# Optimization experiments

Hardware: AMD Instinct MI355X
Metric: run time of the kernel (lower is better)

Reference implementation:

```python
import jax, jax.numpy as jnp
import numpy as np
import math

B, T, D = 4, 1024, 512
H, HD = 8, 64
FF = 2048
L = 2
MEM = 512
S = T + MEM  # src length
EPS = 1e-5


def _sinusoid(positions, dim):
    pos = positions.astype(jnp.float32)[:, None]                      # [P,1]
    div = jnp.exp(jnp.arange(0, dim, 2, dtype=jnp.float32) * (-math.log(10000.0) / dim))
    enc = jnp.zeros((positions.shape[0], dim), jnp.float32)
    enc = enc.at[:, 0::2].set(jnp.sin(pos * div))
    enc = enc.at[:, 1::2].set(jnp.cos(pos * div))
    return enc


def _layer_norm(x, scale, bias):
    m = jnp.mean(x, axis=-1, keepdims=True)
    v = jnp.var(x, axis=-1, keepdims=True)
    return (x - m) / jnp.sqrt(v + EPS) * scale + bias


def _rel_shift(x):
    # x: [T, S, B, H] -> Transformer-XL relative shift
    t, s, b, h = x.shape
    xp = jnp.concatenate([jnp.zeros((t, 1, b, h), x.dtype), x], axis=1)  # [T,S+1,B,H]
    xp = xp.reshape(s + 1, t, b, h)
    return xp[1:].reshape(t, s, b, h)


def setup_inputs() -> dict:
    key = jax.random.key(0)
    ks = jax.random.split(key, 16)
    w = 0.02
    inp = {
        "x": jax.random.normal(ks[0], (B, T, D), jnp.float32),
        "positions": jnp.arange(S - 1, -1, -1, dtype=jnp.int64 if jax.config.jax_enable_x64 else jnp.int32),
        # causal-with-memory mask: query i (src position i+MEM) cannot see src j > i + MEM
        "attn_mask": jnp.arange(S)[None, :] > (jnp.arange(T)[:, None] + MEM),
        "mems": jax.random.normal(ks[1], (L + 1, MEM, B, D), jnp.float32) * 0.5,
        "u_bias": jax.random.normal(ks[2], (H, HD), jnp.float32) * w,
        "v_bias": jax.random.normal(ks[3], (H, HD), jnp.float32) * w,
        "qkv_w": jax.random.normal(ks[4], (L, 3 * H * HD, D), jnp.float32) * w,
        "pos_w": jax.random.normal(ks[5], (L, H * HD, D), jnp.float32) * w,
        "out_w": jax.random.normal(ks[6], (L, D, H * HD), jnp.float32) * w,
        "lin1_w": jax.random.normal(ks[7], (L, FF, D), jnp.float32) * w,
        "lin1_b": jnp.zeros((L, FF), jnp.float32),
        "lin2_w": jax.random.normal(ks[8], (L, D, FF), jnp.float32) * w,
        "lin2_b": jnp.zeros((L, D), jnp.float32),
        "ln1_s": jnp.ones((L, D), jnp.float32),
        "ln1_b": jnp.zeros((L, D), jnp.float32),
        "ln2_s": jnp.ones((L, D), jnp.float32),
        "ln2_b": jnp.zeros((L, D), jnp.float32),
    }
    return inp


def reference(x, positions, attn_mask, mems, u_bias, v_bias, qkv_w, pos_w, out_w,
              lin1_w, lin1_b, lin2_w, lin2_b, ln1_s, ln1_b, ln2_s, ln2_b):
    scale = 1.0 / math.sqrt(D)  # source uses 1/sqrt(embed_dim)
    xs = jnp.swapaxes(x, 0, 1)                       # [T,B,D] (batch_first -> time-first)
    pe = _sinusoid(positions, D)                     # [S,D]
    out = xs
    hiddens = [xs]
    for l in range(L):
        cat = jnp.concatenate([mems[l], out], axis=0)            # [S,B,D]
        qkv = jnp.einsum('sbd,ed->sbe', cat, qkv_w[l])           # [S,B,3*H*HD]
        q, k, v = jnp.split(qkv, 3, axis=-1)
        q = q[-T:].reshape(T, B, H, HD)
        k = k.reshape(S, B, H, HD)
        v = v.reshape(S, B, H, HD)
        r = jnp.einsum('sd,ed->se', pe, pos_w[l]).reshape(S, H, HD)
        content = jnp.einsum('ibnd,jbnd->ijbn', q + u_bias, k)   # [T,S,B,H]
        pos_sc = jnp.einsum('ibnd,jnd->ijbn', q + v_bias, r)     # [T,S,B,H]
        score = (content + _rel_shift(pos_sc)) * scale
        score = jnp.where(attn_mask[:, :, None, None], -jnp.inf, score)
        attn = jax.nn.softmax(score, axis=1)
        ctx = jnp.einsum('ijbn,jbnd->ibnd', attn, v).reshape(T, B, H * HD)
        a_out = jnp.einsum('tbe,de->tbd', ctx, out_w[l])
        h = _layer_norm(out + a_out, ln1_s[l], ln1_b[l])
        ff = jnp.einsum('tbf,df->tbd', jax.nn.relu(jnp.einsum('tbd,fd->tbf', h, lin1_w[l]) + lin1_b[l]), lin2_w[l]) + lin2_b[l]
        out = _layer_norm(h + ff, ln2_s[l], ln2_b[l])
        hiddens.append(out)
    final = jnp.swapaxes(out[-T:], 0, 1)             # [B,T,D]
    new_mems = jax.lax.stop_gradient(jnp.stack(
        [jnp.concatenate([mems[i], hiddens[i]], axis=0)[-MEM:] for i in range(L + 1)], axis=0))
    return final, new_mems
```

## Files before the change

### kernel.cpp

```cpp
#include <hip/hip_runtime.h>

constexpr int BB = 4, TT = 1024, DD = 512, HH = 8, HDIM = 64;
constexpr int FFD = 2048, NLAYER = 2, MM = 512, SS = 1536;
constexpr float LN_EPS = 1e-5f;
constexpr float SCALE = 0.04419417382415922f;

typedef unsigned short u16;
typedef __attribute__((ext_vector_type(8))) short bf16x8;
typedef __attribute__((ext_vector_type(4))) float f32x4;

__device__ __forceinline__ float b2f(u16 u) {
  union { unsigned int i; float f; } c; c.i = ((unsigned int)u) << 16; return c.f;
}
__device__ __forceinline__ u16 f2b(float f) {
  unsigned int x = __builtin_bit_cast(unsigned int, f);
  x += 0x7fffu + ((x >> 16) & 1u);
  return (u16)(x >> 16);
}

__device__ __forceinline__ void dma16(const u16* g, u16* l) {
  __builtin_amdgcn_global_load_lds(
      (const __attribute__((address_space(1))) unsigned int*)g,
      (__attribute__((address_space(3))) unsigned int*)l, 16, 0, 0);
}

constexpr int OFF_X    = 0;
constexpr int OFF_MEMS = 2097152;
constexpr int OFF_UB   = 5242880;
constexpr int OFF_VB   = 5243392;
constexpr int OFF_QKVW = 5243904;
constexpr int OFF_POSW = 6816768;
constexpr int OFF_OUTW = 7341056;
constexpr int OFF_L1W  = 7865344;
constexpr int OFF_L1B  = 9962496;
constexpr int OFF_L2W  = 9966592;
constexpr int OFF_L2B  = 12063744;
constexpr int OFF_LN1S = 12064768;
constexpr int OFF_LN1B = 12065792;
constexpr int OFF_LN2S = 12066816;
constexpr int OFF_LN2B = 12067840;
constexpr int TOT_IN   = 12068864;
constexpr int PE_CNT   = SS * 256;

__global__ void txl_probe(const u16* __restrict__ xr, int* __restrict__ flag) {
  int lane = threadIdx.x;
  int cnt = 0;
  for (int k = 0; k < 8; ++k) {
    u16 u = xr[lane * 8 + k];
    int e = (u >> 7) & 0xFF;
    if (e >= 0xC0) ++cnt;
  }
  for (int o = 32; o; o >>= 1) cnt += __shfl_xor(cnt, o);
  if (lane == 0) *flag = (cnt >= 32) ? 1 : 0;
}

__global__ __launch_bounds__(256) void txl_convert(
    const void* x, const void* mems, const void* ub, const void* vb,
    const void* qkvw, const void* posw, const void* outw,
    const void* l1w, const void* l1b, const void* l2w, const void* l2b,
    const void* ln1s, const void* ln1b, const void* ln2s, const void* ln2b,
    u16* __restrict__ dst, u16* __restrict__ pe, const int* __restrict__ flag) {
  int idx = blockIdx.x * 256 + threadIdx.x;
  if (idx >= TOT_IN) {
    int idx2 = idx - TOT_IN;
    if (idx2 >= PE_CNT) return;
    int p = idx2 >> 8, m = idx2 & 255;
    float posf = (float)(SS - 1 - p);
    float div = expf((float)(2 * m) * (-9.210340371976184f / 512.0f));
    float a = posf * div;
    pe[(size_t)p * DD + 2 * m] = f2b(sinf(a));
    pe[(size_t)p * DD + 2 * m + 1] = f2b(cosf(a));
    return;
  }
  const void* p; int local;
  if      (idx < OFF_MEMS) { p = x;    local = idx; }
  else if (idx < OFF_UB)   { p = mems; local = idx - OFF_MEMS; }
  else if (idx < OFF_VB)   { p = ub;   local = idx - OFF_UB; }
  else if (idx < OFF_QKVW) { p = vb;   local = idx - OFF_VB; }
  else if (idx < OFF_POSW) { p = qkvw; local = idx - OFF_QKVW; }
  else if (idx < OFF_OUTW) { p = posw; local = idx - OFF_POSW; }
  else if (idx < OFF_L1W)  { p = outw; local = idx - OFF_OUTW; }
  else if (idx < OFF_L1B)  { p = l1w;  local = idx - OFF_L1W; }
  else if (idx < OFF_L2W)  { p = l1b;  local = idx - OFF_L1B; }
  else if (idx < OFF_L2B)  { p = l2w;  local = idx - OFF_L2W; }
  else if (idx < OFF_LN1S) { p = l2b;  local = idx - OFF_L2B; }
  else if (idx < OFF_LN1B) { p = ln1s; local = idx - OFF_LN1S; }
  else if (idx < OFF_LN2S) { p = ln1b; local = idx - OFF_LN1B; }
  else if (idx < OFF_LN2B) { p = ln2s; local = idx - OFF_LN2S; }
  else                     { p = ln2b; local = idx - OFF_LN2B; }
  dst[idx] = (*flag) ? f2b(((const float*)p)[local]) : ((const u16*)p)[local];
}

template <int EPI>
__global__ __launch_bounds__(256) void txl_gemm4(const u16* __restrict__ A,
                                                 const u16* __restrict__ B,
                                                 float* __restrict__ C,
                                                 u16* __restrict__ Obf,
                                                 const u16* __restrict__ bias,
                                                 int M, int N, int K, int KS) {
  __shared__ __align__(16) u16 As[2][128 * 32];
  __shared__ __align__(16) u16 Bs[2][128 * 32];
  const int tid = threadIdx.x;
  const int wave = tid >> 6, lane = tid & 63;
  const int wm = (wave & 1) * 64, wn = (wave >> 1) * 64;
  const int m0 = blockIdx.x * 128, n0 = blockIdx.y * 128;
  const int kbeg = blockIdx.z * KS, kend = kbeg + KS;
  const int L15 = lane & 15, quad = lane >> 4;

  auto stage = [&](int k0, int buf) {
    for (int c = 0; c < 2; ++c) {
      int segBase = c * 256 + wave * 64;
      int seg = segBase + lane;
      int row = seg >> 2, q = seg & 3;
      dma16(&A[(size_t)(m0 + row) * K + k0 + q * 8], &As[buf][segBase * 8]);
      dma16(&B[(size_t)(n0 + row) * K + k0 + q * 8], &Bs[buf][segBase * 8]);
    }
  };

  f32x4 acc[4][4] = {};
  stage(kbeg, 0);
  __syncthreads();
  int buf = 0;
  for (int k0 = kbeg; k0 < kend; k0 += 32) {
    if (k0 + 32 < kend) stage(k0 + 32, buf ^ 1);
    bf16x8 af[4], bfr[4];
    for (int t = 0; t < 4; ++t)
      af[t] = *reinterpret_cast<const bf16x8*>(&As[buf][(wm + t * 16 + L15) * 32 + quad * 8]);
    for (int t = 0; t < 4; ++t)
      bfr[t] = *reinterpret_cast<const bf16x8*>(&Bs[buf][(wn + t * 16 + L15) * 32 + quad * 8]);
    for (int tm = 0; tm < 4; ++tm)
      for (int tn = 0; tn < 4; ++tn)
        acc[tm][tn] = __builtin_amdgcn_mfma_f32_16x16x32_bf16(af[tm], bfr[tn], acc[tm][tn], 0, 0, 0);
    buf ^= 1;
    __syncthreads();
  }
  float* Cz = C + (size_t)blockIdx.z * ((size_t)M * N);
#pragma unroll
  for (int tm = 0; tm < 4; ++tm)
#pragma unroll
    for (int tn = 0; tn < 4; ++tn) {
      int col = n0 + wn + tn * 16 + L15;
#pragma unroll
      for (int r = 0; r < 4; ++r) {
        int row = m0 + wm + tm * 16 + quad * 4 + r;
        if (EPI == 0) {
          Cz[(size_t)row * N + col] = acc[tm][tn][r];
        } else {
          float v = acc[tm][tn][r] + b2f(bias[col]);
          Obf[(size_t)row * N + col] = f2b(fmaxf(v, 0.f));
        }
      }
    }
}

__global__ __launch_bounds__(256) void txl_gemm_r(const u16* __restrict__ A,
                                                  const u16* __restrict__ B,
                                                  u16* __restrict__ rb,
                                                  int M, int N, int K) {
  __shared__ __align__(16) u16 As[2][128 * 32];
  __shared__ __align__(16) u16 Bs[2][128 * 32];
  const int tid = threadIdx.x;
  const int wave = tid >> 6, lane = tid & 63;
  const int wm = (wave & 1) * 64, wn = (wave >> 1) * 64;
  const int m0 = blockIdx.x * 128, n0 = blockIdx.y * 128;
  const int L15 = lane & 15, quad = lane >> 4;

  auto stage = [&](int k0, int buf) {
    for (int c = 0; c < 2; ++c) {
      int segBase = c * 256 + wave * 64;
      int seg = segBase + lane;
      int row = seg >> 2, q = seg & 3;
      dma16(&A[(size_t)(m0 + row) * K + k0 + q * 8], &As[buf][segBase * 8]);
      dma16(&B[(size_t)(n0 + row) * K + k0 + q * 8], &Bs[buf][segBase * 8]);
    }
  };

  f32x4 acc[4][4] = {};
  stage(0, 0);
  __syncthreads();
  int buf = 0;
  for (int k0 = 0; k0 < K; k0 += 32) {
    if (k0 + 32 < K) stage(k0 + 32, buf ^ 1);
    bf16x8 af[4], bfr[4];
    for (int t = 0; t < 4; ++t)
      af[t] = *reinterpret_cast<const bf16x8*>(&As[buf][(wm + t * 16 + L15) * 32 + quad * 8]);
    for (int t = 0; t < 4; ++t)
      bfr[t] = *reinterpret_cast<const bf16x8*>(&Bs[buf][(wn + t * 16 + L15) * 32 + quad * 8]);
    for (int tm = 0; tm < 4; ++tm)
      for (int tn = 0; tn < 4; ++tn)
        acc[tm][tn] = __builtin_amdgcn_mfma_f32_16x16x32_bf16(af[tm], bfr[tn], acc[tm][tn], 0, 0, 0);
    buf ^= 1;
    __syncthreads();
  }
#pragma unroll
  for (int tm = 0; tm < 4; ++tm)
#pragma unroll
    for (int tn = 0; tn < 4; ++tn) {
      int col = n0 + wn + tn * 16 + L15;
      int n = col >> 6, d = col & 63;
#pragma unroll
      for (int r = 0; r < 4; ++r) {
        int row = m0 + wm + tm * 16 + quad * 4 + r;
        rb[((size_t)n * SS + row) * HDIM + d] = f2b(acc[tm][tn][r]);
      }
    }
}

__global__ void txl_transpose_in(const u16* __restrict__ x, u16* __restrict__ cur_bf,
                                 float* __restrict__ cur_f, void* __restrict__ outv,
                                 const int* __restrict__ flag) {
  int idx = blockIdx.x * 256 + threadIdx.x;
  if (idx >= BB * TT * DD) return;
  int b = idx >> 19, t = (idx >> 9) & 1023, d = idx & 511;
  u16 v = x[idx];
  size_t o = ((size_t)t * BB + b) * DD + d;
  cur_bf[o] = v; cur_f[o] = b2f(v);
  if (t >= 512) {
    size_t mo = 2097152 + (o - 1048576);
    if (*flag) ((float*)outv)[mo] = b2f(v);
    else       ((u16*)outv)[mo] = v;
  }
}

__global__ __launch_bounds__(256) void txl_qkv_scatter(
    const float* __restrict__ C, const u16* __restrict__ ub, const u16* __restrict__ vb,
    u16* __restrict__ qu, u16* __restrict__ qv, u16* __restrict__ kb) {
  size_t idx = (size_t)blockIdx.x * 256 + threadIdx.x;
  if (idx >= (size_t)SS * BB * 1536) return;
  int e = (int)(idx % 1536);
  if (e >= 1024) return;
  int row = (int)(idx / 1536);
  int s = row >> 2, b = row & 3;
  float val = C[idx];
  if (e < 512) {
    if (s >= MM) {
      int i = s - MM, n = e >> 6, d = e & 63;
      size_t o = ((size_t)(b * HH + n) * TT + i) * HDIM + d;
      qu[o] = f2b(val + b2f(ub[e]));
      qv[o] = f2b(val + b2f(vb[e]));
    }
  } else {
    int e2 = e - 512, n = e2 >> 6, d = e2 & 63;
    kb[((size_t)(b * HH + n) * SS + s) * HDIM + d] = f2b(val);
  }
}

__global__ __launch_bounds__(256) void txl_v_transpose(const float* __restrict__ C,
                                                       u16* __restrict__ vT) {
  __shared__ u16 t[64][68];
  int bx = blockIdx.x;
  int sb = bx >> 5;
  int bn = bx & 31;
  int n = bn & 7, b = bn >> 3;
  int tid = threadIdx.x;
  int s0 = sb * 64;
  {
    int d = tid & 63, sr = tid >> 6;
    for (int i = 0; i < 16; ++i) {
      int s = s0 + sr + i * 4;
      t[sr + i * 4][d] = f2b(C[(size_t)(s * 4 + b) * 1536 + 1024 + n * 64 + d]);
    }
  }
  __syncthreads();
  {
    int s = tid & 63, dr = tid >> 6;
    u16* dst = vT + (size_t)(b * HH + n) * HDIM * SS;
    for (int i = 0; i < 16; ++i) {
      int d2 = dr + i * 4;
      dst[(size_t)d2 * SS + s0 + s] = t[s][d2];
    }
  }
}

__global__ __launch_bounds__(256) void txl_attn9(
    const u16* __restrict__ qu, const u16* __restrict__ qv, const u16* __restrict__ kbuf,
    const u16* __restrict__ vT, const u16* __restrict__ rbuf,
    float* __restrict__ O0, float* __restrict__ O1,
    float* __restrict__ L0, float* __restrict__ L1) {
  __shared__ __align__(16) u16 Kb[2][2048];
  __shared__ __align__(16) u16 Vb[2][2048];
  __shared__ __align__(16) u16 Rr[8][1024];
  __shared__ __align__(16) u16 ps4[4][640];

  const int bx = blockIdx.x;
  const int n = bx & 7;
  const int rest = bx >> 3;
  const int b = rest & 3;
  const int rest2 = rest >> 2;
  const int piece = rest2 >> 4;
  const int st = piece ? (15 - (rest2 & 15)) : (rest2 & 15);
  const int i0b = st * 64;
  const int g0 = 63 - (i0b >> 4);
  const int jcEnd = 18 + 2 * st;
  const int half = 9 + st;
  const int jcBeg = piece ? half : 0;
  const int jcLim = piece ? jcEnd : half;
  const int gB = g0 + 2 * jcBeg;

  const int tid = threadIdx.x, w = tid >> 6, lane = tid & 63;
  const int L15 = lane & 15, quad = lane >> 4;
  const int i0w = i0b + 16 * w;
  const int bh = b * HH + n;

  const u16* kB = kbuf + (size_t)bh * SS * HDIM;
  const u16* rB = rbuf + (size_t)n * SS * HDIM;
  const u16* vB = vT + (size_t)bh * HDIM * SS;

  const u16* quB = qu + ((size_t)bh * TT + i0w) * HDIM;
  const u16* qvB = qv + ((size_t)bh * TT + i0w) * HDIM;
  bf16x8 aqu[2], aqv[2];
  for (int c = 0; c < 2; ++c) {
    aqu[c] = *reinterpret_cast<const bf16x8*>(&quB[(size_t)L15 * HDIM + c * 32 + quad * 8]);
    aqv[c] = *reinterpret_cast<const bf16x8*>(&qvB[(size_t)L15 * HDIM + c * 32 + quad * 8]);
  }

  u16* ps = &ps4[w][0];

  auto stageK = [&](int jc) {
    const u16* src = kB + (size_t)(jc * 32 + (lane & 31)) * HDIM + (2 * w + (lane >> 5)) * 8;
    dma16(src, &Kb[jc & 1][512 * w]);
  };
  auto stageV = [&](int jc) {
    const u16* src = vB + (size_t)lane * SS + jc * 32 + 8 * w;
    dma16(src, &Vb[jc & 1][512 * w]);
  };
  auto stageRslab = [&](int slab) {
    int rrow = slab * 16 + (lane & 15);
    rrow = (rrow > SS - 1) ? (SS - 1) : rrow;
    const u16* s0 = rB + (size_t)rrow * HDIM + (lane >> 4) * 8;
    dma16(s0, &Rr[slab & 7][0]);
    dma16(s0 + 32, &Rr[slab & 7][512]);
  };
  auto rfrag = [&](int slab, int h) {
    return *reinterpret_cast<const bf16x8*>(&Rr[slab & 7][((quad + 4 * h) * 16 + L15) * 8]);
  };

  stageK(jcBeg); stageV(jcBeg);
  stageRslab(gB - 3 + w);
  if (w < 2) stageRslab(gB + 1 + w);
  __syncthreads();

  f32x4 pT0 = {};
  pT0 = __builtin_amdgcn_mfma_f32_16x16x32_bf16(aqv[0], rfrag(gB - w, 0), pT0, 0, 0, 0);
  pT0 = __builtin_amdgcn_mfma_f32_16x16x32_bf16(aqv[1], rfrag(gB - w, 1), pT0, 0, 0, 0);

  float l_lane[4] = {0.f, 0.f, 0.f, 0.f};
  f32x4 Oacc[4] = {};

  for (int jc = jcBeg; jc < jcLim; ++jc) {
    if (jc + 1 < jcLim) {
      stageK(jc + 1); stageV(jc + 1);
      if (w < 2) stageRslab(g0 + 3 + 2 * jc + w);
    }
    const int hslot = jc & 1, j0 = jc * 32;
    bf16x8 k00 = *reinterpret_cast<const bf16x8*>(&Kb[hslot][((quad) * 32 + L15) * 8]);
    bf16x8 k01 = *reinterpret_cast<const bf16x8*>(&Kb[hslot][((quad + 4) * 32 + L15) * 8]);
    bf16x8 k10 = *reinterpret_cast<const bf16x8*>(&Kb[hslot][((quad) * 32 + 16 + L15) * 8]);
    bf16x8 k11 = *reinterpret_cast<const bf16x8*>(&Kb[hslot][((quad + 4) * 32 + 16 + L15) * 8]);
    f32x4 s0v = {}, s1v = {};
    s0v = __builtin_amdgcn_mfma_f32_16x16x32_bf16(aqu[0], k00, s0v, 0, 0, 0);
    s0v = __builtin_amdgcn_mfma_f32_16x16x32_bf16(aqu[1], k01, s0v, 0, 0, 0);
    s1v = __builtin_amdgcn_mfma_f32_16x16x32_bf16(aqu[0], k10, s1v, 0, 0, 0);
    s1v = __builtin_amdgcn_mfma_f32_16x16x32_bf16(aqu[1], k11, s1v, 0, 0, 0);
    const int sl1 = g0 - w + 2 * jc + 1;
    f32x4 pT1 = {}, pT2 = {};
    pT1 = __builtin_amdgcn_mfma_f32_16x16x32_bf16(aqv[0], rfrag(sl1, 0), pT1, 0, 0, 0);
    pT1 = __builtin_amdgcn_mfma_f32_16x16x32_bf16(aqv[1], rfrag(sl1, 1), pT1, 0, 0, 0);
    pT2 = __builtin_amdgcn_mfma_f32_16x16x32_bf16(aqv[0], rfrag(sl1 + 1, 0), pT2, 0, 0, 0);
    pT2 = __builtin_amdgcn_mfma_f32_16x16x32_bf16(aqv[1], rfrag(sl1 + 1, 1), pT2, 0, 0, 0);
    for (int r = 0; r < 4; ++r) {
      int ii = quad * 4 + r;
      int i = i0w + ii;
      int c = 15 + L15 - ii;
      int srcLane = (quad << 4) | (c & 15);
      float a0 = __shfl(pT0[r], srcLane);
      float a1 = __shfl(pT1[r], srcLane);
      float b1v = __shfl(pT2[r], srcLane);
      float sv0 = s0v[r] + ((c < 16) ? a0 : a1);
      float sv1 = s1v[r] + ((c < 16) ? a1 : b1v);
      sv0 = (j0 + L15 <= i + MM) ? sv0 : -3e38f;
      sv1 = (j0 + 16 + L15 <= i + MM) ? sv1 : -3e38f;
      float e0 = __expf(sv0 * SCALE);
      float e1 = __expf(sv1 * SCALE);
      l_lane[r] += e0 + e1;
      int row = ii * 40;
      ps[row + L15] = f2b(e0);
      ps[row + 16 + L15] = f2b(e1);
    }
    bf16x8 ap = *reinterpret_cast<const bf16x8*>(&ps[L15 * 40 + quad * 8]);
    bf16x8 v0 = *reinterpret_cast<const bf16x8*>(&Vb[hslot][(quad * 64 + L15) * 8]);
    bf16x8 v1 = *reinterpret_cast<const bf16x8*>(&Vb[hslot][(quad * 64 + 16 + L15) * 8]);
    bf16x8 v2 = *reinterpret_cast<const bf16x8*>(&Vb[hslot][(quad * 64 + 32 + L15) * 8]);
    bf16x8 v3 = *reinterpret_cast<const bf16x8*>(&Vb[hslot][(quad * 64 + 48 + L15) * 8]);
    Oacc[0] = __builtin_amdgcn_mfma_f32_16x16x32_bf16(ap, v0, Oacc[0], 0, 0, 0);
    Oacc[1] = __builtin_amdgcn_mfma_f32_16x16x32_bf16(ap, v1, Oacc[1], 0, 0, 0);
    Oacc[2] = __builtin_amdgcn_mfma_f32_16x16x32_bf16(ap, v2, Oacc[2], 0, 0, 0);
    Oacc[3] = __builtin_amdgcn_mfma_f32_16x16x32_bf16(ap, v3, Oacc[3], 0, 0, 0);
    pT0 = pT2;
    __syncthreads();
  }

  float lsum[4];
  for (int r = 0; r < 4; ++r) {
    float s = l_lane[r];
    for (int o = 1; o < 16; o <<= 1) s += __shfl_xor(s, o);
    lsum[r] = s;
  }
  float* Op = piece ? O1 : O0;
  float* Lp = piece ? L1 : L0;
  for (int tn = 0; tn < 4; ++tn)
    for (int r = 0; r < 4; ++r) {
      int ii = quad * 4 + r;
      Op[((size_t)(i0w + ii) * BB + b) * DD + n * HDIM + tn * 16 + L15] = Oacc[tn][r];
    }
  if (L15 == 0)
    for (int r = 0; r < 4; ++r)
      Lp[(size_t)bh * TT + i0w + quad * 4 + r] = lsum[r];
}

__global__ void txl_attn_merge(const float* __restrict__ O0, const float* __restrict__ O1,
                               const float* __restrict__ L0, const float* __restrict__ L1,
                               u16* __restrict__ ctx) {
  int o = blockIdx.x * 256 + threadIdx.x;
  if (o >= BB * TT * DD) return;
  int i = o >> 11, b = (o >> 9) & 3, e = o & 511, n = e >> 6;
  size_t li = (size_t)(b * HH + n) * TT + i;
  float l = L0[li] + L1[li];
  ctx[o] = f2b((O0[o] + O1[o]) / l);
}

__global__ __launch_bounds__(256) void txl_ln(
    const float* __restrict__ gout, int nparts, const u16* __restrict__ bias,
    const float* __restrict__ resid, const u16* __restrict__ gam, const u16* __restrict__ bet,
    u16* __restrict__ ybf, float* __restrict__ yf,
    void* __restrict__ outv, int off, void* __restrict__ finalv,
    const int* __restrict__ flag) {
  const int row = blockIdx.x, tid = threadIdx.x;
  const int lane = tid & 63, wave = tid >> 6;
  __shared__ float red[4];
  size_t base = (size_t)row * DD;
  float x0 = resid[base + tid];
  float x1 = resid[base + tid + 256];
  for (int p = 0; p < nparts; ++p) {
    x0 += gout[(size_t)p * 2097152 + base + tid];
    x1 += gout[(size_t)p * 2097152 + base + tid + 256];
  }
  if (bias) { x0 += b2f(bias[tid]); x1 += b2f(bias[tid + 256]); }
  float s = x0 + x1;
  for (int o = 32; o; o >>= 1) s += __shfl_xor(s, o);
  if (lane == 0) red[wave] = s;
  __syncthreads();
  float mean = (red[0] + red[1] + red[2] + red[3]) * (1.f / DD);
  __syncthreads();
  float d0 = x0 - mean, d1 = x1 - mean;
  float q = d0 * d0 + d1 * d1;
  for (int o = 32; o; o >>= 1) q += __shfl_xor(q, o);
  if (lane == 0) red[wave] = q;
  __syncthreads();
  float var = (red[0] + red[1] + red[2] + red[3]) * (1.f / DD);
  float rstd = rsqrtf(var + LN_EPS);
  float y0 = d0 * rstd * b2f(gam[tid]) + b2f(bet[tid]);
  float y1 = d1 * rstd * b2f(gam[tid + 256]) + b2f(bet[tid + 256]);
  u16 u0 = f2b(y0), u1 = f2b(y1);
  ybf[base + tid] = u0;
  ybf[base + tid + 256] = u1;
  yf[base + tid] = y0;
  yf[base + tid + 256] = y1;
  if (outv && row >= 2048) {
    size_t mo = (size_t)off + (size_t)(row - 2048) * DD;
    if (*flag) {
      ((float*)outv)[mo + tid] = y0;
      ((float*)outv)[mo + tid + 256] = y1;
    } else {
      ((u16*)outv)[mo + tid] = u0;
      ((u16*)outv)[mo + tid + 256] = u1;
    }
  }
  if (finalv) {
    int t = row >> 2, b = row & 3;
    size_t fo = ((size_t)b * TT + t) * DD;
    if (*flag) {
      ((float*)finalv)[fo + tid] = y0;
      ((float*)finalv)[fo + tid + 256] = y1;
    } else {
      ((u16*)finalv)[fo + tid] = u0;
      ((u16*)finalv)[fo + tid + 256] = u1;
    }
  }
}

constexpr size_t WS_CUR_F  = 0;
constexpr size_t WS_CAT    = 8388608;
constexpr size_t WS_CBUF   = 14680064;
constexpr size_t WS_QU     = 52428800;
constexpr size_t WS_QV     = 56623104;
constexpr size_t WS_K      = 60817408;
constexpr size_t WS_VT     = 67108864;
constexpr size_t WS_R      = 73400320;
constexpr size_t WS_PE     = 74973184;
constexpr size_t WS_CTX    = 76546048;
constexpr size_t WS_HBF    = 80740352;
constexpr size_t WS_HF     = 84934656;
constexpr size_t WS_FF1    = 93323264;
constexpr size_t WS_CURBF  = 110100480;
constexpr size_t WS_CIN    = 114294784;
constexpr size_t WS_FLAG   = 138432512;
constexpr size_t WS_TOTAL  = 138432576;
constexpr size_t WS_OB0 = WS_CBUF;
constexpr size_t WS_OB1 = WS_CBUF + 8388608;
constexpr size_t WS_LB0 = WS_CBUF + 16777216;
constexpr size_t WS_LB1 = WS_CBUF + 16908288;

extern "C" void kernel_launch(void* const* d_in, const int* in_sizes, int n_in,
                              void* d_out, int out_size, void* d_ws, size_t ws_size,
                              hipStream_t stream) {
  (void)in_sizes; (void)n_in;

  if (ws_size < WS_TOTAL) {
    hipMemsetAsync(d_out, 0, (size_t)out_size * 2, stream);
    return;
  }
  char* ws = (char*)d_ws;
  float* cur_f  = (float*)(ws + WS_CUR_F);
  u16*   cat    = (u16*)(ws + WS_CAT);
  float* Cbuf   = (float*)(ws + WS_CBUF);
  float* Ob0    = (float*)(ws + WS_OB0);
  float* Ob1    = (float*)(ws + WS_OB1);
  float* Lb0    = (float*)(ws + WS_LB0);
  float* Lb1    = (float*)(ws + WS_LB1);
  u16*   qu     = (u16*)(ws + WS_QU);
  u16*   qv     = (u16*)(ws + WS_QV);
  u16*   kb     = (u16*)(ws + WS_K);
  u16*   vT     = (u16*)(ws + WS_VT);
  u16*   rb     = (u16*)(ws + WS_R);
  u16*   pe     = (u16*)(ws + WS_PE);
  u16*   ctx    = (u16*)(ws + WS_CTX);
  u16*   hbf    = (u16*)(ws + WS_HBF);
  float* hf     = (float*)(ws + WS_HF);
  u16*   ff1    = (u16*)(ws + WS_FF1);
  u16*   cur_bf = (u16*)(ws + WS_CURBF);
  u16*   cin    = (u16*)(ws + WS_CIN);
  int*   flag   = (int*)(ws + WS_FLAG);

  txl_probe<<<1, 64, 0, stream>>>((const u16*)d_in[0], flag);
  txl_convert<<<48680, 256, 0, stream>>>(
      d_in[0], d_in[3], d_in[4], d_in[5], d_in[6], d_in[7], d_in[8],
      d_in[9], d_in[10], d_in[11], d_in[12], d_in[13], d_in[14], d_in[15], d_in[16],
      cin, pe, flag);

  const u16* ub = cin + OFF_UB;
  const u16* vb = cin + OFF_VB;

  txl_transpose_in<<<8192, 256, 0, stream>>>(cin + OFF_X, cur_bf, cur_f, d_out, flag);

  for (int l = 0; l < NLAYER; ++l) {
    hipMemcpyAsync(cat, cin + OFF_MEMS + (size_t)l * 1048576, 2097152,
                   hipMemcpyDeviceToDevice, stream);
    hipMemcpyAsync(cat + 1048576, cur_bf, 4194304, hipMemcpyDeviceToDevice, stream);
    txl_gemm4<0><<<dim3(48, 12, 1), 256, 0, stream>>>(
        cat, cin + OFF_QKVW + (size_t)l * 786432, Cbuf, nullptr, nullptr, 6144, 1536, 512, 512);
    txl_qkv_scatter<<<36864, 256, 0, stream>>>(Cbuf, ub, vb, qu, qv, kb);
    txl_v_transpose<<<768, 256, 0, stream>>>(Cbuf, vT);
    txl_gemm_r<<<dim3(12, 4), 256, 0, stream>>>(
        pe, cin + OFF_POSW + (size_t)l * 262144, rb, 1536, 512, 512);
    txl_attn9<<<1024, 256, 0, stream>>>(qu, qv, kb, vT, rb, Ob0, Ob1, Lb0, Lb1);
    txl_attn_merge<<<8192, 256, 0, stream>>>(Ob0, Ob1, Lb0, Lb1, ctx);
    txl_gemm4<0><<<dim3(32, 4, 2), 256, 0, stream>>>(
        ctx, cin + OFF_OUTW + (size_t)l * 262144, Cbuf, nullptr, nullptr, 4096, 512, 512, 256);
    txl_ln<<<4096, 256, 0, stream>>>(Cbuf, 2, nullptr, cur_f,
                                     cin + OFF_LN1S + l * 512, cin + OFF_LN1B + l * 512,
                                     hbf, hf, nullptr, 0, nullptr, flag);
    txl_gemm4<1><<<dim3(32, 16, 1), 256, 0, stream>>>(
        hbf, cin + OFF_L1W + (size_t)l * 1048576, nullptr, ff1,
        cin + OFF_L1B + l * 2048, 4096, 2048, 512, 512);
    txl_gemm4<0><<<dim3(32, 4, 4), 256, 0, stream>>>(
        ff1, cin + OFF_L2W + (size_t)l * 1048576, Cbuf, nullptr, nullptr, 4096, 512, 2048, 512);
    txl_ln<<<4096, 256, 0, stream>>>(Cbuf, 4, cin + OFF_L2B + l * 512, hf,
                                     cin + OFF_LN2S + l * 512, cin + OFF_LN2B + l * 512,
                                     cur_bf, cur_f, d_out, 2097152 + (l + 1) * 1048576,
                                     (l == NLAYER - 1) ? d_out : nullptr, flag);
  }
}
```

Before: 476.0 us.

## Drop concat copies, batch positional GEMMs, merge QKV scatter with V transpose

The QKV GEMM now reads its A operand from two base pointers (memory rows, then current hidden rows), so the two device-to-device copies that built the concatenated buffer are removed. The positional projection for both layers is computed once up front in a single launch using a z grid dimension. The QKV scatter and V transpose kernels are merged into one launch that also skips the unused V columns in the scatter part. Together these cut launches and memory traffic, at the cost of a larger rel-pos buffer and extra pointer selection in the GEMM.

```diff
diff --git a/kernel.cpp b/kernel.cpp
--- a/kernel.cpp
+++ b/kernel.cpp
@@ -93,6 +93,7 @@
 
 template <int EPI>
 __global__ __launch_bounds__(256) void txl_gemm4(const u16* __restrict__ A,
+                                                 const u16* __restrict__ A2, int msplit,
                                                  const u16* __restrict__ B,
                                                  float* __restrict__ C,
                                                  u16* __restrict__ Obf,
@@ -106,13 +107,14 @@
   const int m0 = blockIdx.x * 128, n0 = blockIdx.y * 128;
   const int kbeg = blockIdx.z * KS, kend = kbeg + KS;
   const int L15 = lane & 15, quad = lane >> 4;
+  const u16* Abase = (m0 < msplit) ? (A + (size_t)m0 * K) : (A2 + (size_t)(m0 - msplit) * K);
 
   auto stage = [&](int k0, int buf) {
     for (int c = 0; c < 2; ++c) {
       int segBase = c * 256 + wave * 64;
       int seg = segBase + lane;
       int row = seg >> 2, q = seg & 3;
-      dma16(&A[(size_t)(m0 + row) * K + k0 + q * 8], &As[buf][segBase * 8]);
+      dma16(&Abase[(size_t)row * K + k0 + q * 8], &As[buf][segBase * 8]);
       dma16(&B[(size_t)(n0 + row) * K + k0 + q * 8], &Bs[buf][segBase * 8]);
     }
   };
@@ -164,6 +166,8 @@
   const int wm = (wave & 1) * 64, wn = (wave >> 1) * 64;
   const int m0 = blockIdx.x * 128, n0 = blockIdx.y * 128;
   const int L15 = lane & 15, quad = lane >> 4;
+  const u16* Bz = B + (size_t)blockIdx.z * 262144;
+  u16* rbz = rb + (size_t)blockIdx.z * 786432;
 
   auto stage = [&](int k0, int buf) {
     for (int c = 0; c < 2; ++c) {
@@ -171,7 +175,7 @@
       int seg = segBase + lane;
       int row = seg >> 2, q = seg & 3;
       dma16(&A[(size_t)(m0 + row) * K + k0 + q * 8], &As[buf][segBase * 8]);
-      dma16(&B[(size_t)(n0 + row) * K + k0 + q * 8], &Bs[buf][segBase * 8]);
+      dma16(&Bz[(size_t)(n0 + row) * K + k0 + q * 8], &Bs[buf][segBase * 8]);
     }
   };
 
@@ -201,7 +205,7 @@
 #pragma unroll
       for (int r = 0; r < 4; ++r) {
         int row = m0 + wm + tm * 16 + quad * 4 + r;
-        rb[((size_t)n * SS + row) * HDIM + d] = f2b(acc[tm][tn][r]);
+        rbz[((size_t)n * SS + row) * HDIM + d] = f2b(acc[tm][tn][r]);
       }
     }
 }
@@ -222,16 +226,40 @@
   }
 }
 
-__global__ __launch_bounds__(256) void txl_qkv_scatter(
+__global__ __launch_bounds__(256) void txl_qkv_post(
     const float* __restrict__ C, const u16* __restrict__ ub, const u16* __restrict__ vb,
-    u16* __restrict__ qu, u16* __restrict__ qv, u16* __restrict__ kb) {
-  size_t idx = (size_t)blockIdx.x * 256 + threadIdx.x;
-  if (idx >= (size_t)SS * BB * 1536) return;
-  int e = (int)(idx % 1536);
-  if (e >= 1024) return;
-  int row = (int)(idx / 1536);
+    u16* __restrict__ qu, u16* __restrict__ qv, u16* __restrict__ kb,
+    u16* __restrict__ vT) {
+  __shared__ u16 t[64][68];
+  const int bx = blockIdx.x;
+  const int tid = threadIdx.x;
+  if (bx < 768) {
+    int sb = bx >> 5;
+    int bn = bx & 31;
+    int n = bn & 7, b = bn >> 3;
+    int s0 = sb * 64;
+    {
+      int d = tid & 63, sr = tid >> 6;
+      for (int i = 0; i < 16; ++i) {
+        int s = s0 + sr + i * 4;
+        t[sr + i * 4][d] = f2b(C[(size_t)(s * 4 + b) * 1536 + 1024 + n * 64 + d]);
+      }
+    }
+    __syncthreads();
+    {
+      int s = tid & 63, dr = tid >> 6;
+      u16* dst = vT + (size_t)(b * HH + n) * HDIM * SS;
+      for (int i = 0; i < 16; ++i) {
+        int d2 = dr + i * 4;
+        dst[(size_t)d2 * SS + s0 + s] = t[s][d2];
+      }
+    }
+    return;
+  }
+  int idx = (bx - 768) * 256 + tid;
+  int row = idx >> 10, e = idx & 1023;
   int s = row >> 2, b = row & 3;
-  float val = C[idx];
+  float val = C[(size_t)row * 1536 + e];
   if (e < 512) {
     if (s >= MM) {
       int i = s - MM, n = e >> 6, d = e & 63;
@@ -242,33 +270,6 @@
   } else {
     int e2 = e - 512, n = e2 >> 6, d = e2 & 63;
     kb[((size_t)(b * HH + n) * SS + s) * HDIM + d] = f2b(val);
-  }
-}
-
-__global__ __launch_bounds__(256) void txl_v_transpose(const float* __restrict__ C,
-                                                       u16* __restrict__ vT) {
-  __shared__ u16 t[64][68];
-  int bx = blockIdx.x;
-  int sb = bx >> 5;
-  int bn = bx & 31;
-  int n = bn & 7, b = bn >> 3;
-  int tid = threadIdx.x;
-  int s0 = sb * 64;
-  {
-    int d = tid & 63, sr = tid >> 6;
-    for (int i = 0; i < 16; ++i) {
-      int s = s0 + sr + i * 4;
-      t[sr + i * 4][d] = f2b(C[(size_t)(s * 4 + b) * 1536 + 1024 + n * 64 + d]);
-    }
-  }
-  __syncthreads();
-  {
-    int s = tid & 63, dr = tid >> 6;
-    u16* dst = vT + (size_t)(b * HH + n) * HDIM * SS;
-    for (int i = 0; i < 16; ++i) {
-      int d2 = dr + i * 4;
-      dst[(size_t)d2 * SS + s0 + s] = t[s][d2];
-    }
   }
 }
 
@@ -490,7 +491,7 @@
 }
 
 constexpr size_t WS_CUR_F  = 0;
-constexpr size_t WS_CAT    = 8388608;
+constexpr size_t WS_RB2    = 8388608;
 constexpr size_t WS_CBUF   = 14680064;
 constexpr size_t WS_QU     = 52428800;
 constexpr size_t WS_QV     = 56623104;
@@ -522,7 +523,7 @@
   }
   char* ws = (char*)d_ws;
   float* cur_f  = (float*)(ws + WS_CUR_F);
-  u16*   cat    = (u16*)(ws + WS_CAT);
+  u16*   rb2    = (u16*)(ws + WS_RB2);
   float* Cbuf   = (float*)(ws + WS_CBUF);
   float* Ob0    = (float*)(ws + WS_OB0);
   float* Ob1    = (float*)(ws + WS_OB1);
@@ -532,7 +533,6 @@
   u16*   qv     = (u16*)(ws + WS_QV);
   u16*   kb     = (u16*)(ws + WS_K);
   u16*   vT     = (u16*)(ws + WS_VT);
-  u16*   rb     = (u16*)(ws + WS_R);
   u16*   pe     = (u16*)(ws + WS_PE);
   u16*   ctx    = (u16*)(ws + WS_CTX);
   u16*   hbf    = (u16*)(ws + WS_HBF);
@@ -551,30 +551,30 @@
   const u16* ub = cin + OFF_UB;
   const u16* vb = cin + OFF_VB;
 
+  txl_gemm_r<<<dim3(12, 4, 2), 256, 0, stream>>>(
+      pe, cin + OFF_POSW, rb2, 1536, 512, 512);
   txl_transpose_in<<<8192, 256, 0, stream>>>(cin + OFF_X, cur_bf, cur_f, d_out, flag);
 
   for (int l = 0; l < NLAYER; ++l) {
-    hipMemcpyAsync(cat, cin + OFF_MEMS + (size_t)l * 1048576, 2097152,
-                   hipMemcpyDeviceToDevice, stream);
-    hipMemcpyAsync(cat + 1048576, cur_bf, 4194304, hipMemcpyDeviceToDevice, stream);
     txl_gemm4<0><<<dim3(48, 12, 1), 256, 0, stream>>>(
-        cat, cin + OFF_QKVW + (size_t)l * 786432, Cbuf, nullptr, nullptr, 6144, 1536, 512, 512);
-    txl_qkv_scatter<<<36864, 256, 0, stream>>>(Cbuf, ub, vb, qu, qv, kb);
-    txl_v_transpose<<<768, 256, 0, stream>>>(Cbuf, vT);
-    txl_gemm_r<<<dim3(12, 4), 256, 0, stream>>>(
-        pe, cin + OFF_POSW + (size_t)l * 262144, rb, 1536, 512, 512);
-    txl_attn9<<<1024, 256, 0, stream>>>(qu, qv, kb, vT, rb, Ob0, Ob1, Lb0, Lb1);
+        cin + OFF_MEMS + (size_t)l * 1048576, cur_bf, 2048,
+        cin + OFF_QKVW + (size_t)l * 786432, Cbuf, nullptr, nullptr, 6144, 1536, 512, 512);
+    txl_qkv_post<<<25344, 256, 0, stream>>>(Cbuf, ub, vb, qu, qv, kb, vT);
+    txl_attn9<<<1024, 256, 0, stream>>>(qu, qv, kb, vT, rb2 + (size_t)l * 786432,
+                                        Ob0, Ob1, Lb0, Lb1);
     txl_attn_merge<<<8192, 256, 0, stream>>>(Ob0, Ob1, Lb0, Lb1, ctx);
     txl_gemm4<0><<<dim3(32, 4, 2), 256, 0, stream>>>(
-        ctx, cin + OFF_OUTW + (size_t)l * 262144, Cbuf, nullptr, nullptr, 4096, 512, 512, 256);
+        ctx, ctx, 1 << 30, cin + OFF_OUTW + (size_t)l * 262144, Cbuf,
+        nullptr, nullptr, 4096, 512, 512, 256);
     txl_ln<<<4096, 256, 0, stream>>>(Cbuf, 2, nullptr, cur_f,
                                      cin + OFF_LN1S + l * 512, cin + OFF_LN1B + l * 512,
                                      hbf, hf, nullptr, 0, nullptr, flag);
     txl_gemm4<1><<<dim3(32, 16, 1), 256, 0, stream>>>(
-        hbf, cin + OFF_L1W + (size_t)l * 1048576, nullptr, ff1,
-        cin + OFF_L1B + l * 2048, 4096, 2048, 512, 512);
+        hbf, hbf, 1 << 30, cin + OFF_L1W + (size_t)l * 1048576, nullptr,
+        ff1, cin + OFF_L1B + l * 2048, 4096, 2048, 512, 512);
     txl_gemm4<0><<<dim3(32, 4, 4), 256, 0, stream>>>(
-        ff1, cin + OFF_L2W + (size_t)l * 1048576, Cbuf, nullptr, nullptr, 4096, 512, 2048, 512);
+        ff1, ff1, 1 << 30, cin + OFF_L2W + (size_t)l * 1048576, Cbuf,
+        nullptr, nullptr, 4096, 512, 2048, 512);
     txl_ln<<<4096, 256, 0, stream>>>(Cbuf, 4, cin + OFF_L2B + l * 512, hf,
                                      cin + OFF_LN2S + l * 512, cin + OFF_LN2B + l * 512,
                                      cur_bf, cur_f, d_out, 2097152 + (l + 1) * 1048576,
```

Result: faster. 448.6 us (-5.8%).
